# Performance work log

Measured on AMD Instinct MI355X. Metric: run time of the kernel, lower is better.

## Reference

```python
import jax, jax.numpy as jnp
import numpy as np

D_MODEL = 256
N_BINS = 11
# standard KNRM kernels: exact-match bin (mu=1, sigma=1e-3) + 10 soft bins
MUS = jnp.array([1.0, 0.9, 0.7, 0.5, 0.3, 0.1, -0.1, -0.3, -0.5, -0.7, -0.9], dtype=jnp.float32)
SIGMAS = jnp.array([1e-3] + [0.1] * 10, dtype=jnp.float32)


def _l2norm(x, eps=1e-10):
    # F.normalize(p=2, eps=1e-10): x / max(||x||, eps)
    n = jnp.sqrt(jnp.sum(x * x, axis=-1, keepdims=True))
    return x / jnp.maximum(n, eps)


def setup_inputs() -> dict:
    key = jax.random.key(0)
    ks = jax.random.split(key, 10)
    B, NB, Q, T, D = 64, 8, 32, 256, D_MODEL
    return {
        "word_atten": jax.random.uniform(ks[0], (B, NB, Q), dtype=jnp.float32),
        "hq": jax.random.normal(ks[1], (B, NB, Q, D), dtype=jnp.float32),
        "can": jax.random.normal(ks[2], (B, T, D), dtype=jnp.float32),
        "rep": jax.random.normal(ks[3], (B, NB, D), dtype=jnp.float32),
        "rep_cur": jax.random.normal(ks[4], (B, D), dtype=jnp.float32),
        "mask_hq": jnp.ones((B, NB, Q), dtype=jnp.float32),
        "mask_can": jnp.ones((B, T), dtype=jnp.float32),
        "mask_session": jnp.ones((B, NB), dtype=jnp.float32),
        "W_dense": jax.random.normal(ks[5], (N_BINS, 1), dtype=jnp.float32) * 0.3,
        "b_dense": jnp.zeros((1,), dtype=jnp.float32),
        "W_att": jax.random.normal(ks[6], (D, D), dtype=jnp.float32) * (1.0 / np.sqrt(D)),
        "b_att": jnp.zeros((D,), dtype=jnp.float32),
    }


def reference(word_atten, hq, can, rep, rep_cur, mask_hq, mask_can, mask_session,
              W_dense, b_dense, W_att, b_att):
    # cosine-similarity matrix: [B, NB, Q, T]
    hq_n = _l2norm(hq)
    can_n = _l2norm(can)
    matrix = jnp.einsum("bnqd,btd->bnqt", hq_n, can_n)

    # Gaussian kernel soft-binning: expand to [B, NB, Q, T, N_BINS]
    diff = matrix[..., None] - MUS  # broadcast over bins
    kern = jnp.exp(-(diff * diff) / (2.0 * SIGMAS * SIGMAS))
    kern = kern * mask_can[:, None, None, :, None]  # mask doc tokens
    pooling_sum = jnp.sum(kern, axis=3)  # [B, NB, Q, N_BINS]

    log_pool = jnp.log(jnp.clip(pooling_sum, 1e-10)) * 0.01
    log_pool = log_pool * mask_hq[..., None] * word_atten[..., None]
    pooled = jnp.sum(log_pool, axis=2)  # [B, NB, N_BINS]

    pooled = pooled * mask_session[..., None]

    # attention over session blocks (AttendAttention): scaled dot with projected current rep
    q = rep_cur @ W_att + b_att  # [B, D]
    scores = jnp.einsum("bnd,bd->bn", rep, q) / np.sqrt(D_MODEL).astype(np.float32)
    scores = jnp.where(mask_session > 0, scores, -1e9)
    attn = jax.nn.softmax(scores, axis=-1)  # [B, NB]

    score = jnp.tanh(pooled @ W_dense + b_dense).squeeze(-1)  # [B, NB]
    return jnp.sum(score * attn, axis=1)  # [B]
```

## Files before the change

kernel.cpp:

```cpp
#include <hip/hip_runtime.h>

#define B_ 64
#define NB_ 8
#define Q_ 32
#define T_ 256
#define D_ 256
#define NBINS 11

typedef __attribute__((ext_vector_type(8))) short bf16x8;
typedef __attribute__((ext_vector_type(4))) float f32x4;
typedef unsigned short ushort_t;
typedef unsigned int uint_t;

#define CANH_OFF 0u
#define CANL_OFF 8388608u

__device__ inline ushort_t bf16_rnd(float f) {
  uint_t u = __float_as_uint(f);
  return (ushort_t)((u + 0x8000u) >> 16);
}
__device__ inline uint_t pack2(ushort_t a, ushort_t b) {
  return (uint_t)a | ((uint_t)b << 16);
}

__global__ __launch_bounds__(256) void split_kernel(
    const float* __restrict__ can, uint4* __restrict__ canH,
    uint4* __restrict__ canL, float* __restrict__ out) {
  __shared__ __align__(16) ushort_t sm_hi[32 * 264];
  __shared__ __align__(16) ushort_t sm_lo[32 * 264];
  int blk = blockIdx.x;
  int tid = threadIdx.x;
  if (tid == 0 && blk < B_) out[blk] = 0.0f;
  int b = blk >> 3, ch = blk & 7;
  const float* src = can + ((size_t)b * T_ + ch * 32) * D_;
  int tilebase = b * 16 + ch * 2;

#pragma unroll
  for (int it = 0; it < 4; it++) {
    int flat = it * 2048 + tid * 8;
    int row = flat >> 8, col = flat & 255;
    const float* p = src + row * D_ + col;
    float4 x = reinterpret_cast<const float4*>(p)[0];
    float4 y = reinterpret_cast<const float4*>(p)[1];
    float s = x.x * x.x + x.y * x.y + x.z * x.z + x.w * x.w +
              y.x * y.x + y.y * y.y + y.z * y.z + y.w * y.w;
    s += __shfl_xor(s, 1);
    s += __shfl_xor(s, 2);
    s += __shfl_xor(s, 4);
    s += __shfl_xor(s, 8);
    s += __shfl_xor(s, 16);
    float inv = 1.0f / fmaxf(sqrtf(s), 1e-10f);
    float v[8] = {x.x, x.y, x.z, x.w, y.x, y.y, y.z, y.w};
    ushort_t h[8], l[8];
#pragma unroll
    for (int j = 0; j < 8; j++) {
      float sv = v[j] * inv;
      h[j] = bf16_rnd(sv);
      float hf = __uint_as_float(((uint_t)h[j]) << 16);
      l[j] = bf16_rnd(sv - hf);
    }
    uint4 ph = {pack2(h[0], h[1]), pack2(h[2], h[3]), pack2(h[4], h[5]),
                pack2(h[6], h[7])};
    uint4 pl = {pack2(l[0], l[1]), pack2(l[2], l[3]), pack2(l[4], l[5]),
                pack2(l[6], l[7])};
    *reinterpret_cast<uint4*>(&sm_hi[row * 264 + col]) = ph;
    *reinterpret_cast<uint4*>(&sm_lo[row * 264 + col]) = pl;
  }
  __syncthreads();
  int wv = tid >> 6, lane = tid & 63;
  int tl = wv >> 1, part = wv & 1;
  int lq = lane & 15, lk = lane >> 4;
  const ushort_t* smp = part ? sm_lo : sm_hi;
  uint4* dst = part ? canL : canH;
#pragma unroll
  for (int kk = 0; kk < 8; kk++) {
    const ushort_t* a = &smp[(tl * 16 + lq) * 264 + kk * 32 + lk * 8];
    dst[((size_t)(tilebase + tl) * 8 + kk) * 64 + lane] =
        *reinterpret_cast<const uint4*>(a);
  }
}

__global__ __launch_bounds__(256, 2) void pool_kernel(
    const float* __restrict__ hq, const uint4* __restrict__ canH,
    const uint4* __restrict__ canL, const float* __restrict__ mask_can,
    const float* __restrict__ word_atten, const float* __restrict__ mask_hq,
    const float* __restrict__ rep, const float* __restrict__ rep_cur,
    const float* __restrict__ mask_session, const float* __restrict__ W_dense,
    const float* __restrict__ b_dense, const float* __restrict__ W_att,
    const float* __restrict__ b_att, float* __restrict__ out) {
  __shared__ float smbuf[1331];
  float* partial = smbuf;
  float* lp_sm = smbuf + 704;
  float* qproj = smbuf + 1056;
  float* scores_sm = smbuf + 1312;
  float* pooled_sm = smbuf + 1320;

  const float mus[NBINS] = {1.0f, 0.9f, 0.7f, 0.5f, 0.3f, 0.1f,
                            -0.1f, -0.3f, -0.5f, -0.7f, -0.9f};
  const float nis2[NBINS] = {-5.0e5f, -50.f, -50.f, -50.f, -50.f, -50.f,
                             -50.f, -50.f, -50.f, -50.f, -50.f};

  int i = blockIdx.x;
  int b = i & 63;
  int nb = i >> 6;
  int outb = b * NB_ + nb;
  int tid = threadIdx.x;
  int wv = tid >> 6, lane = tid & 63;
  int lq = lane & 15, lk = lane >> 4;
  int mtile = wv & 1, tq = wv >> 1;

  const float* arow =
      hq + (size_t)outb * (Q_ * D_) + (size_t)(mtile * 16 + lq) * D_;
  float sumsq = 0.f;
#pragma unroll
  for (int kk = 0; kk < 8; kk++) {
    const float* p = arow + kk * 32 + lk * 8;
    float4 x = reinterpret_cast<const float4*>(p)[0];
    float4 y = reinterpret_cast<const float4*>(p)[1];
    sumsq += x.x * x.x + x.y * x.y + x.z * x.z + x.w * x.w +
             y.x * y.x + y.y * y.y + y.z * y.z + y.w * y.w;
  }
  sumsq += __shfl_xor(sumsq, 16);
  sumsq += __shfl_xor(sumsq, 32);
  float ainv = 1.0f / fmaxf(sqrtf(sumsq), 1e-10f);

  bf16x8 ah[8], al[8];
#pragma unroll
  for (int kk = 0; kk < 8; kk++) {
    const float* p = arow + kk * 32 + lk * 8;
    float4 x = reinterpret_cast<const float4*>(p)[0];
    float4 y = reinterpret_cast<const float4*>(p)[1];
    float v[8] = {x.x, x.y, x.z, x.w, y.x, y.y, y.z, y.w};
    union { bf16x8 v8; ushort_t u[8]; } H, L;
#pragma unroll
    for (int j = 0; j < 8; j++) {
      float s = v[j] * ainv;
      ushort_t h = bf16_rnd(s);
      float hf = __uint_as_float(((uint_t)h) << 16);
      H.u[j] = h;
      L.u[j] = bf16_rnd(s - hf);
    }
    ah[kk] = H.v8;
    al[kk] = L.v8;
  }

  float binacc[4][NBINS];
#pragma unroll
  for (int r = 0; r < 4; r++)
#pragma unroll
    for (int j = 0; j < NBINS; j++) binacc[r][j] = 0.0f;

  f32x4 accPrev;
  float mkPrev = 0.0f;

  {
    int tt = tq * 8;
    size_t bbase = (size_t)(b * 16 + tt) * 8 * 64 + lane;
    f32x4 acc = {0.f, 0.f, 0.f, 0.f};
#pragma unroll
    for (int kk = 0; kk < 8; kk++) {
      bf16x8 bh = *reinterpret_cast<const bf16x8*>(&canH[bbase + kk * 64]);
      bf16x8 bl = *reinterpret_cast<const bf16x8*>(&canL[bbase + kk * 64]);
      acc = __builtin_amdgcn_mfma_f32_16x16x32_bf16(ah[kk], bh, acc, 0, 0, 0);
      acc = __builtin_amdgcn_mfma_f32_16x16x32_bf16(al[kk], bh, acc, 0, 0, 0);
      acc = __builtin_amdgcn_mfma_f32_16x16x32_bf16(ah[kk], bl, acc, 0, 0, 0);
    }
    accPrev = acc;
    mkPrev = mask_can[b * T_ + tt * 16 + lq];
  }

  for (int ti = 1; ti < 8; ti++) {
    int tt = tq * 8 + ti;
    size_t bbase = (size_t)(b * 16 + tt) * 8 * 64 + lane;
    bf16x8 bh[8], bl[8];
#pragma unroll
    for (int kk = 0; kk < 8; kk++) {
      bh[kk] = *reinterpret_cast<const bf16x8*>(&canH[bbase + kk * 64]);
      bl[kk] = *reinterpret_cast<const bf16x8*>(&canL[bbase + kk * 64]);
    }
#pragma unroll
    for (int r = 0; r < 4; r++) {
      float v0 = accPrev[r];
#pragma unroll
      for (int j = 0; j < NBINS; j++) {
        float d0 = v0 - mus[j];
        binacc[r][j] += mkPrev * __expf(d0 * d0 * nis2[j]);
      }
    }
    f32x4 acc = {0.f, 0.f, 0.f, 0.f};
#pragma unroll
    for (int kk = 0; kk < 8; kk++) {
      acc = __builtin_amdgcn_mfma_f32_16x16x32_bf16(ah[kk], bh[kk], acc, 0, 0, 0);
      acc = __builtin_amdgcn_mfma_f32_16x16x32_bf16(al[kk], bh[kk], acc, 0, 0, 0);
      acc = __builtin_amdgcn_mfma_f32_16x16x32_bf16(ah[kk], bl[kk], acc, 0, 0, 0);
    }
    accPrev = acc;
    mkPrev = mask_can[b * T_ + tt * 16 + lq];
  }
#pragma unroll
  for (int r = 0; r < 4; r++) {
    float v0 = accPrev[r];
#pragma unroll
    for (int j = 0; j < NBINS; j++) {
      float d0 = v0 - mus[j];
      binacc[r][j] += mkPrev * __expf(d0 * d0 * nis2[j]);
    }
  }

#pragma unroll
  for (int r = 0; r < 4; r++)
#pragma unroll
    for (int j = 0; j < NBINS; j++) {
      float v = binacc[r][j];
      v += __shfl_xor(v, 1);
      v += __shfl_xor(v, 2);
      v += __shfl_xor(v, 4);
      v += __shfl_xor(v, 8);
      binacc[r][j] = v;
    }
  if (lq == 0) {
#pragma unroll
    for (int r = 0; r < 4; r++)
#pragma unroll
      for (int j = 0; j < NBINS; j++)
        partial[(wv * 16 + lk * 4 + r) * NBINS + j] = binacc[r][j];
  }
  __syncthreads();

  for (int idx = tid; idx < Q_ * NBINS; idx += 256) {
    int q = idx / NBINS;
    int j = idx - q * NBINS;
    int m = q >> 4, r16 = q & 15;
    float sum = partial[(m * 16 + r16) * NBINS + j] +
                partial[((2 + m) * 16 + r16) * NBINS + j];
    float wa = word_atten[outb * Q_ + q] * mask_hq[outb * Q_ + q];
    lp_sm[idx] = logf(fmaxf(sum, 1e-10f)) * 0.01f * wa;
  }

  {
    const float* rc = rep_cur + b * D_;
    float acc2 = b_att[tid];
    for (int k = 0; k < D_; k++) acc2 += rc[k] * W_att[k * D_ + tid];
    qproj[tid] = acc2;
  }
  __syncthreads();

  if (tid < NBINS) {
    float s = 0.f;
#pragma unroll
    for (int q = 0; q < Q_; q++) s += lp_sm[q * NBINS + tid];
    pooled_sm[tid] = s;
  }

  for (int nn = wv; nn < NB_; nn += 4) {
    const float* rp = rep + ((size_t)b * NB_ + nn) * D_;
    float4 r4 = reinterpret_cast<const float4*>(rp)[lane];
    float4 q4 = *reinterpret_cast<float4*>(&qproj[lane * 4]);
    float s = r4.x * q4.x + r4.y * q4.y + r4.z * q4.z + r4.w * q4.w;
#pragma unroll
    for (int off = 32; off > 0; off >>= 1) s += __shfl_down(s, off);
    if (lane == 0) scores_sm[nn] = s * 0.0625f;
  }
  __syncthreads();

  if (tid == 0) {
    float sc[NB_];
    float mx = -1e30f;
    for (int nn = 0; nn < NB_; nn++) {
      float s = (mask_session[b * NB_ + nn] > 0.f) ? scores_sm[nn] : -1e9f;
      sc[nn] = s;
      mx = fmaxf(mx, s);
    }
    float den = 0.f;
    for (int nn = 0; nn < NB_; nn++) {
      sc[nn] = __expf(sc[nn] - mx);
      den += sc[nn];
    }
    float ms = mask_session[b * NB_ + nb];
    float pw = b_dense[0];
#pragma unroll
    for (int j = 0; j < NBINS; j++) pw += pooled_sm[j] * ms * W_dense[j];
    float res = tanhf(pw) * (sc[nb] / den);
    atomicAdd(&out[b], res);
  }
}

extern "C" void kernel_launch(void* const* d_in, const int* in_sizes, int n_in,
                              void* d_out, int out_size, void* d_ws,
                              size_t ws_size, hipStream_t stream) {
  const float* word_atten = (const float*)d_in[0];
  const float* hq = (const float*)d_in[1];
  const float* can = (const float*)d_in[2];
  const float* rep = (const float*)d_in[3];
  const float* rep_cur = (const float*)d_in[4];
  const float* mask_hq = (const float*)d_in[5];
  const float* mask_can = (const float*)d_in[6];
  const float* mask_session = (const float*)d_in[7];
  const float* W_dense = (const float*)d_in[8];
  const float* b_dense = (const float*)d_in[9];
  const float* W_att = (const float*)d_in[10];
  const float* b_att = (const float*)d_in[11];
  float* out = (float*)d_out;

  char* ws = (char*)d_ws;
  uint4* canH = (uint4*)(ws + CANH_OFF);
  uint4* canL = (uint4*)(ws + CANL_OFF);

  hipLaunchKernelGGL(split_kernel, dim3(512), dim3(256), 0, stream, can, canH,
                     canL, out);
  hipLaunchKernelGGL(pool_kernel, dim3(B_ * NB_), dim3(256), 0, stream, hq,
                     canH, canL, mask_can, word_atten, mask_hq, rep, rep_cur,
                     mask_session, W_dense, b_dense, W_att, b_att, out);
}
```

Measured before the change: 127.1 us.

## Factor Gaussian bins via exponential recurrence and hoist attention to split kernel

Result: slower. 149.5 us (+17.6%).

```diff
diff --git a/kernel.cpp b/kernel.cpp
--- a/kernel.cpp
+++ b/kernel.cpp
@@ -14,6 +14,7 @@
 
 #define CANH_OFF 0u
 #define CANL_OFF 8388608u
+#define ATTN_OFF 16777216u
 
 __device__ inline ushort_t bf16_rnd(float f) {
   uint_t u = __float_as_uint(f);
@@ -23,11 +24,40 @@
   return (uint_t)a | ((uint_t)b << 16);
 }
 
+__device__ inline void kern_bins(float v, float mk, float* acc) {
+  float d0 = v - 1.0f;
+  acc[0] += mk * exp2f(d0 * d0 * -721347.52f);
+  float t = v - 0.1f;
+  float K = mk * exp2f(t * t * -72.134752f);
+  acc[5] += K;
+  float x = v * 28.853901f;
+  float eu = exp2f(x);
+  float ed = exp2f(-x);
+  const float E4 = 1.8315639e-2f;
+  const float E8 = 3.3546262e-4f;
+  const float E12 = 6.1442124e-6f;
+  const float E16 = 1.1253517e-7f;
+  float kd = K * ed;        acc[6] += kd;
+  kd = kd * ed * E4;        acc[7] += kd;
+  kd = kd * ed * E8;        acc[8] += kd;
+  kd = kd * ed * E12;       acc[9] += kd;
+  kd = kd * ed * E16;       acc[10] += kd;
+  float ku = K * eu * E4;   acc[4] += ku;
+  ku = ku * eu * E8;        acc[3] += ku;
+  ku = ku * eu * E12;       acc[2] += ku;
+  ku = ku * eu * E16;       acc[1] += ku;
+}
+
 __global__ __launch_bounds__(256) void split_kernel(
     const float* __restrict__ can, uint4* __restrict__ canH,
-    uint4* __restrict__ canL, float* __restrict__ out) {
+    uint4* __restrict__ canL, const float* __restrict__ rep,
+    const float* __restrict__ rep_cur, const float* __restrict__ mask_session,
+    const float* __restrict__ W_att, const float* __restrict__ b_att,
+    float* __restrict__ attn_out, float* __restrict__ out) {
   __shared__ __align__(16) ushort_t sm_hi[32 * 264];
   __shared__ __align__(16) ushort_t sm_lo[32 * 264];
+  __shared__ float qp_sm[256];
+  __shared__ float sc_sm[8];
   int blk = blockIdx.x;
   int tid = threadIdx.x;
   if (tid == 0 && blk < B_) out[blk] = 0.0f;
@@ -78,27 +108,55 @@
     dst[((size_t)(tilebase + tl) * 8 + kk) * 64 + lane] =
         *reinterpret_cast<const uint4*>(a);
   }
+
+  if (ch == 0) {
+    const float* rc = rep_cur + b * D_;
+    float acc2 = b_att[tid];
+#pragma unroll 8
+    for (int k = 0; k < D_; k++) acc2 += rc[k] * W_att[(size_t)k * D_ + tid];
+    qp_sm[tid] = acc2;
+    __syncthreads();
+    for (int nn = wv; nn < NB_; nn += 4) {
+      const float* rp = rep + ((size_t)b * NB_ + nn) * D_;
+      float4 r4 = reinterpret_cast<const float4*>(rp)[lane];
+      float4 q4 = *reinterpret_cast<const float4*>(&qp_sm[lane * 4]);
+      float s = r4.x * q4.x + r4.y * q4.y + r4.z * q4.z + r4.w * q4.w;
+#pragma unroll
+      for (int off = 32; off > 0; off >>= 1) s += __shfl_down(s, off);
+      if (lane == 0) sc_sm[nn] = s * 0.0625f;
+    }
+    __syncthreads();
+    if (tid == 0) {
+      float sc[NB_];
+      float mx = -1e30f;
+      for (int nn = 0; nn < NB_; nn++) {
+        float s = (mask_session[b * NB_ + nn] > 0.f) ? sc_sm[nn] : -1e9f;
+        sc[nn] = s;
+        mx = fmaxf(mx, s);
+      }
+      float den = 0.f;
+      for (int nn = 0; nn < NB_; nn++) {
+        sc[nn] = __expf(sc[nn] - mx);
+        den += sc[nn];
+      }
+      float invd = 1.0f / den;
+      for (int nn = 0; nn < NB_; nn++)
+        attn_out[b * NB_ + nn] = sc[nn] * invd;
+    }
+  }
 }
 
 __global__ __launch_bounds__(256, 2) void pool_kernel(
     const float* __restrict__ hq, const uint4* __restrict__ canH,
     const uint4* __restrict__ canL, const float* __restrict__ mask_can,
     const float* __restrict__ word_atten, const float* __restrict__ mask_hq,
-    const float* __restrict__ rep, const float* __restrict__ rep_cur,
     const float* __restrict__ mask_session, const float* __restrict__ W_dense,
-    const float* __restrict__ b_dense, const float* __restrict__ W_att,
-    const float* __restrict__ b_att, float* __restrict__ out) {
-  __shared__ float smbuf[1331];
+    const float* __restrict__ b_dense, const float* __restrict__ attn_ws,
+    float* __restrict__ out) {
+  __shared__ float smbuf[1067];
   float* partial = smbuf;
   float* lp_sm = smbuf + 704;
-  float* qproj = smbuf + 1056;
-  float* scores_sm = smbuf + 1312;
-  float* pooled_sm = smbuf + 1320;
-
-  const float mus[NBINS] = {1.0f, 0.9f, 0.7f, 0.5f, 0.3f, 0.1f,
-                            -0.1f, -0.3f, -0.5f, -0.7f, -0.9f};
-  const float nis2[NBINS] = {-5.0e5f, -50.f, -50.f, -50.f, -50.f, -50.f,
-                             -50.f, -50.f, -50.f, -50.f, -50.f};
+  float* pooled_sm = smbuf + 1056;
 
   int i = blockIdx.x;
   int b = i & 63;
@@ -179,14 +237,7 @@
       bl[kk] = *reinterpret_cast<const bf16x8*>(&canL[bbase + kk * 64]);
     }
 #pragma unroll
-    for (int r = 0; r < 4; r++) {
-      float v0 = accPrev[r];
-#pragma unroll
-      for (int j = 0; j < NBINS; j++) {
-        float d0 = v0 - mus[j];
-        binacc[r][j] += mkPrev * __expf(d0 * d0 * nis2[j]);
-      }
-    }
+    for (int r = 0; r < 4; r++) kern_bins(accPrev[r], mkPrev, binacc[r]);
     f32x4 acc = {0.f, 0.f, 0.f, 0.f};
 #pragma unroll
     for (int kk = 0; kk < 8; kk++) {
@@ -198,14 +249,8 @@
     mkPrev = mask_can[b * T_ + tt * 16 + lq];
   }
 #pragma unroll
-  for (int r = 0; r < 4; r++) {
-    float v0 = accPrev[r];
-#pragma unroll
-    for (int j = 0; j < NBINS; j++) {
-      float d0 = v0 - mus[j];
-      binacc[r][j] += mkPrev * __expf(d0 * d0 * nis2[j]);
-    }
-  }
+  for (int r = 0; r < 4; r++)
+    kern_bins(accPrev[r], mkPrev, binacc[r]);
 
 #pragma unroll
   for (int r = 0; r < 4; r++)
@@ -236,13 +281,6 @@
     float wa = word_atten[outb * Q_ + q] * mask_hq[outb * Q_ + q];
     lp_sm[idx] = logf(fmaxf(sum, 1e-10f)) * 0.01f * wa;
   }
-
-  {
-    const float* rc = rep_cur + b * D_;
-    float acc2 = b_att[tid];
-    for (int k = 0; k < D_; k++) acc2 += rc[k] * W_att[k * D_ + tid];
-    qproj[tid] = acc2;
-  }
   __syncthreads();
 
   if (tid < NBINS) {
@@ -251,36 +289,12 @@
     for (int q = 0; q < Q_; q++) s += lp_sm[q * NBINS + tid];
     pooled_sm[tid] = s;
   }
-
-  for (int nn = wv; nn < NB_; nn += 4) {
-    const float* rp = rep + ((size_t)b * NB_ + nn) * D_;
-    float4 r4 = reinterpret_cast<const float4*>(rp)[lane];
-    float4 q4 = *reinterpret_cast<float4*>(&qproj[lane * 4]);
-    float s = r4.x * q4.x + r4.y * q4.y + r4.z * q4.z + r4.w * q4.w;
-#pragma unroll
-    for (int off = 32; off > 0; off >>= 1) s += __shfl_down(s, off);
-    if (lane == 0) scores_sm[nn] = s * 0.0625f;
-  }
-  __syncthreads();
-
   if (tid == 0) {
-    float sc[NB_];
-    float mx = -1e30f;
-    for (int nn = 0; nn < NB_; nn++) {
-      float s = (mask_session[b * NB_ + nn] > 0.f) ? scores_sm[nn] : -1e9f;
-      sc[nn] = s;
-      mx = fmaxf(mx, s);
-    }
-    float den = 0.f;
-    for (int nn = 0; nn < NB_; nn++) {
-      sc[nn] = __expf(sc[nn] - mx);
-      den += sc[nn];
-    }
-    float ms = mask_session[b * NB_ + nb];
+    float ms = mask_session[outb];
     float pw = b_dense[0];
 #pragma unroll
     for (int j = 0; j < NBINS; j++) pw += pooled_sm[j] * ms * W_dense[j];
-    float res = tanhf(pw) * (sc[nb] / den);
+    float res = tanhf(pw) * attn_ws[outb];
     atomicAdd(&out[b], res);
   }
 }
@@ -305,10 +319,12 @@
   char* ws = (char*)d_ws;
   uint4* canH = (uint4*)(ws + CANH_OFF);
   uint4* canL = (uint4*)(ws + CANL_OFF);
+  float* attn_ws = (float*)(ws + ATTN_OFF);
 
   hipLaunchKernelGGL(split_kernel, dim3(512), dim3(256), 0, stream, can, canH,
-                     canL, out);
+                     canL, rep, rep_cur, mask_session, W_att, b_att, attn_ws,
+                     out);
   hipLaunchKernelGGL(pool_kernel, dim3(B_ * NB_), dim3(256), 0, stream, hq,
-                     canH, canL, mask_can, word_atten, mask_hq, rep, rep_cur,
-                     mask_session, W_dense, b_dense, W_att, b_att, out);
-}
+                     canH, canL, mask_can, word_atten, mask_hq, mask_session,
+                     W_dense, b_dense, attn_ws, out);
+}
```

## Split pooling across T chunks, pre-split hq, add finish kernel

Applied to the files above, without the earlier changes.

Result: slower. 139.7 us (+10.0%).

```diff
diff --git a/kernel.cpp b/kernel.cpp
--- a/kernel.cpp
+++ b/kernel.cpp
@@ -14,6 +14,9 @@
 
 #define CANH_OFF 0u
 #define CANL_OFF 8388608u
+#define HQH_OFF 16777216u
+#define HQL_OFF 25165824u
+#define PSUM_OFF 33554432u
 
 __device__ inline ushort_t bf16_rnd(float f) {
   uint_t u = __float_as_uint(f);
@@ -23,17 +26,46 @@
   return (uint_t)a | ((uint_t)b << 16);
 }
 
+__device__ inline void bins_acc(f32x4 acc, float mk, float binacc[4][NBINS]) {
+  const float mus[NBINS] = {1.0f, 0.9f, 0.7f, 0.5f, 0.3f, 0.1f,
+                            -0.1f, -0.3f, -0.5f, -0.7f, -0.9f};
+  const float nis2[NBINS] = {-5.0e5f, -50.f, -50.f, -50.f, -50.f, -50.f,
+                             -50.f, -50.f, -50.f, -50.f, -50.f};
+#pragma unroll
+  for (int r = 0; r < 4; r++) {
+    float v0 = acc[r];
+#pragma unroll
+    for (int j = 0; j < NBINS; j++) {
+      float d0 = v0 - mus[j];
+      binacc[r][j] += mk * __expf(d0 * d0 * nis2[j]);
+    }
+  }
+}
+
 __global__ __launch_bounds__(256) void split_kernel(
-    const float* __restrict__ can, uint4* __restrict__ canH,
-    uint4* __restrict__ canL, float* __restrict__ out) {
+    const float* __restrict__ can, const float* __restrict__ hq,
+    uint4* __restrict__ canH, uint4* __restrict__ canL,
+    uint4* __restrict__ hqH, uint4* __restrict__ hqL) {
   __shared__ __align__(16) ushort_t sm_hi[32 * 264];
   __shared__ __align__(16) ushort_t sm_lo[32 * 264];
   int blk = blockIdx.x;
   int tid = threadIdx.x;
-  if (tid == 0 && blk < B_) out[blk] = 0.0f;
-  int b = blk >> 3, ch = blk & 7;
-  const float* src = can + ((size_t)b * T_ + ch * 32) * D_;
-  int tilebase = b * 16 + ch * 2;
+  const float* src;
+  uint4 *dH, *dL;
+  int tilebase;
+  if (blk < 512) {
+    int b = blk >> 3, ch = blk & 7;
+    src = can + ((size_t)b * T_ + ch * 32) * D_;
+    dH = canH;
+    dL = canL;
+    tilebase = b * 16 + ch * 2;
+  } else {
+    int outb = blk - 512;
+    src = hq + (size_t)outb * (Q_ * D_);
+    dH = hqH;
+    dL = hqL;
+    tilebase = outb * 2;
+  }
 
 #pragma unroll
   for (int it = 0; it < 4; it++) {
@@ -71,7 +103,7 @@
   int tl = wv >> 1, part = wv & 1;
   int lq = lane & 15, lk = lane >> 4;
   const ushort_t* smp = part ? sm_lo : sm_hi;
-  uint4* dst = part ? canL : canH;
+  uint4* dst = part ? dL : dH;
 #pragma unroll
   for (int kk = 0; kk < 8; kk++) {
     const ushort_t* a = &smp[(tl * 16 + lq) * 264 + kk * 32 + lk * 8];
@@ -81,68 +113,32 @@
 }
 
 __global__ __launch_bounds__(256, 2) void pool_kernel(
-    const float* __restrict__ hq, const uint4* __restrict__ canH,
-    const uint4* __restrict__ canL, const float* __restrict__ mask_can,
-    const float* __restrict__ word_atten, const float* __restrict__ mask_hq,
-    const float* __restrict__ rep, const float* __restrict__ rep_cur,
-    const float* __restrict__ mask_session, const float* __restrict__ W_dense,
-    const float* __restrict__ b_dense, const float* __restrict__ W_att,
-    const float* __restrict__ b_att, float* __restrict__ out) {
-  __shared__ float smbuf[1331];
-  float* partial = smbuf;
-  float* lp_sm = smbuf + 704;
-  float* qproj = smbuf + 1056;
-  float* scores_sm = smbuf + 1312;
-  float* pooled_sm = smbuf + 1320;
-
-  const float mus[NBINS] = {1.0f, 0.9f, 0.7f, 0.5f, 0.3f, 0.1f,
-                            -0.1f, -0.3f, -0.5f, -0.7f, -0.9f};
-  const float nis2[NBINS] = {-5.0e5f, -50.f, -50.f, -50.f, -50.f, -50.f,
-                             -50.f, -50.f, -50.f, -50.f, -50.f};
+    const uint4* __restrict__ hqH, const uint4* __restrict__ hqL,
+    const uint4* __restrict__ canH, const uint4* __restrict__ canL,
+    const float* __restrict__ mask_can, float* __restrict__ psum) {
+  __shared__ float partial[4 * 16 * NBINS];
 
   int i = blockIdx.x;
   int b = i & 63;
-  int nb = i >> 6;
+  int rest = i >> 6;
+  int nb = rest & 7, ts = rest >> 3;
   int outb = b * NB_ + nb;
   int tid = threadIdx.x;
   int wv = tid >> 6, lane = tid & 63;
   int lq = lane & 15, lk = lane >> 4;
   int mtile = wv & 1, tq = wv >> 1;
 
-  const float* arow =
-      hq + (size_t)outb * (Q_ * D_) + (size_t)(mtile * 16 + lq) * D_;
-  float sumsq = 0.f;
-#pragma unroll
-  for (int kk = 0; kk < 8; kk++) {
-    const float* p = arow + kk * 32 + lk * 8;
-    float4 x = reinterpret_cast<const float4*>(p)[0];
-    float4 y = reinterpret_cast<const float4*>(p)[1];
-    sumsq += x.x * x.x + x.y * x.y + x.z * x.z + x.w * x.w +
-             y.x * y.x + y.y * y.y + y.z * y.z + y.w * y.w;
-  }
-  sumsq += __shfl_xor(sumsq, 16);
-  sumsq += __shfl_xor(sumsq, 32);
-  float ainv = 1.0f / fmaxf(sqrtf(sumsq), 1e-10f);
-
   bf16x8 ah[8], al[8];
-#pragma unroll
-  for (int kk = 0; kk < 8; kk++) {
-    const float* p = arow + kk * 32 + lk * 8;
-    float4 x = reinterpret_cast<const float4*>(p)[0];
-    float4 y = reinterpret_cast<const float4*>(p)[1];
-    float v[8] = {x.x, x.y, x.z, x.w, y.x, y.y, y.z, y.w};
-    union { bf16x8 v8; ushort_t u[8]; } H, L;
-#pragma unroll
-    for (int j = 0; j < 8; j++) {
-      float s = v[j] * ainv;
-      ushort_t h = bf16_rnd(s);
-      float hf = __uint_as_float(((uint_t)h) << 16);
-      H.u[j] = h;
-      L.u[j] = bf16_rnd(s - hf);
-    }
-    ah[kk] = H.v8;
-    al[kk] = L.v8;
-  }
+  size_t abase = (size_t)(outb * 2 + mtile) * 512 + lane;
+#pragma unroll
+  for (int kk = 0; kk < 8; kk++) {
+    ah[kk] = *reinterpret_cast<const bf16x8*>(&hqH[abase + kk * 64]);
+    al[kk] = *reinterpret_cast<const bf16x8*>(&hqL[abase + kk * 64]);
+  }
+
+  int t0 = ts * 4 + tq * 2;
+  float mk0 = mask_can[b * T_ + (t0 + 0) * 16 + lq];
+  float mk1 = mask_can[b * T_ + (t0 + 1) * 16 + lq];
 
   float binacc[4][NBINS];
 #pragma unroll
@@ -150,62 +146,31 @@
 #pragma unroll
     for (int j = 0; j < NBINS; j++) binacc[r][j] = 0.0f;
 
-  f32x4 accPrev;
-  float mkPrev = 0.0f;
-
-  {
-    int tt = tq * 8;
-    size_t bbase = (size_t)(b * 16 + tt) * 8 * 64 + lane;
-    f32x4 acc = {0.f, 0.f, 0.f, 0.f};
-#pragma unroll
-    for (int kk = 0; kk < 8; kk++) {
-      bf16x8 bh = *reinterpret_cast<const bf16x8*>(&canH[bbase + kk * 64]);
-      bf16x8 bl = *reinterpret_cast<const bf16x8*>(&canL[bbase + kk * 64]);
-      acc = __builtin_amdgcn_mfma_f32_16x16x32_bf16(ah[kk], bh, acc, 0, 0, 0);
-      acc = __builtin_amdgcn_mfma_f32_16x16x32_bf16(al[kk], bh, acc, 0, 0, 0);
-      acc = __builtin_amdgcn_mfma_f32_16x16x32_bf16(ah[kk], bl, acc, 0, 0, 0);
-    }
-    accPrev = acc;
-    mkPrev = mask_can[b * T_ + tt * 16 + lq];
-  }
-
-  for (int ti = 1; ti < 8; ti++) {
-    int tt = tq * 8 + ti;
-    size_t bbase = (size_t)(b * 16 + tt) * 8 * 64 + lane;
-    bf16x8 bh[8], bl[8];
-#pragma unroll
-    for (int kk = 0; kk < 8; kk++) {
-      bh[kk] = *reinterpret_cast<const bf16x8*>(&canH[bbase + kk * 64]);
-      bl[kk] = *reinterpret_cast<const bf16x8*>(&canL[bbase + kk * 64]);
-    }
-#pragma unroll
-    for (int r = 0; r < 4; r++) {
-      float v0 = accPrev[r];
-#pragma unroll
-      for (int j = 0; j < NBINS; j++) {
-        float d0 = v0 - mus[j];
-        binacc[r][j] += mkPrev * __expf(d0 * d0 * nis2[j]);
-      }
-    }
-    f32x4 acc = {0.f, 0.f, 0.f, 0.f};
-#pragma unroll
-    for (int kk = 0; kk < 8; kk++) {
-      acc = __builtin_amdgcn_mfma_f32_16x16x32_bf16(ah[kk], bh[kk], acc, 0, 0, 0);
-      acc = __builtin_amdgcn_mfma_f32_16x16x32_bf16(al[kk], bh[kk], acc, 0, 0, 0);
-      acc = __builtin_amdgcn_mfma_f32_16x16x32_bf16(ah[kk], bl[kk], acc, 0, 0, 0);
-    }
-    accPrev = acc;
-    mkPrev = mask_can[b * T_ + tt * 16 + lq];
-  }
-#pragma unroll
-  for (int r = 0; r < 4; r++) {
-    float v0 = accPrev[r];
-#pragma unroll
-    for (int j = 0; j < NBINS; j++) {
-      float d0 = v0 - mus[j];
-      binacc[r][j] += mkPrev * __expf(d0 * d0 * nis2[j]);
-    }
-  }
+  size_t bbase = (size_t)(b * 16 + t0) * 512 + lane;
+  f32x4 acc0 = {0.f, 0.f, 0.f, 0.f};
+#pragma unroll
+  for (int kk = 0; kk < 8; kk++) {
+    bf16x8 bh = *reinterpret_cast<const bf16x8*>(&canH[bbase + kk * 64]);
+    bf16x8 bl = *reinterpret_cast<const bf16x8*>(&canL[bbase + kk * 64]);
+    acc0 = __builtin_amdgcn_mfma_f32_16x16x32_bf16(ah[kk], bh, acc0, 0, 0, 0);
+    acc0 = __builtin_amdgcn_mfma_f32_16x16x32_bf16(al[kk], bh, acc0, 0, 0, 0);
+    acc0 = __builtin_amdgcn_mfma_f32_16x16x32_bf16(ah[kk], bl, acc0, 0, 0, 0);
+  }
+  bf16x8 bh1[8], bl1[8];
+#pragma unroll
+  for (int kk = 0; kk < 8; kk++) {
+    bh1[kk] = *reinterpret_cast<const bf16x8*>(&canH[bbase + 512 + kk * 64]);
+    bl1[kk] = *reinterpret_cast<const bf16x8*>(&canL[bbase + 512 + kk * 64]);
+  }
+  bins_acc(acc0, mk0, binacc);
+  f32x4 acc1 = {0.f, 0.f, 0.f, 0.f};
+#pragma unroll
+  for (int kk = 0; kk < 8; kk++) {
+    acc1 = __builtin_amdgcn_mfma_f32_16x16x32_bf16(ah[kk], bh1[kk], acc1, 0, 0, 0);
+    acc1 = __builtin_amdgcn_mfma_f32_16x16x32_bf16(al[kk], bh1[kk], acc1, 0, 0, 0);
+    acc1 = __builtin_amdgcn_mfma_f32_16x16x32_bf16(ah[kk], bl1[kk], acc1, 0, 0, 0);
+  }
+  bins_acc(acc1, mk1, binacc);
 
 #pragma unroll
   for (int r = 0; r < 4; r++)
@@ -231,24 +196,60 @@
     int q = idx / NBINS;
     int j = idx - q * NBINS;
     int m = q >> 4, r16 = q & 15;
-    float sum = partial[(m * 16 + r16) * NBINS + j] +
-                partial[((2 + m) * 16 + r16) * NBINS + j];
-    float wa = word_atten[outb * Q_ + q] * mask_hq[outb * Q_ + q];
-    lp_sm[idx] = logf(fmaxf(sum, 1e-10f)) * 0.01f * wa;
-  }
-
-  {
+    float s = partial[((0 + m) * 16 + r16) * NBINS + j] +
+              partial[((2 + m) * 16 + r16) * NBINS + j];
+    psum[((size_t)(outb * 4 + ts)) * (Q_ * NBINS) + idx] = s;
+  }
+}
+
+__global__ __launch_bounds__(256) void finish_kernel(
+    const float* __restrict__ psum, const float* __restrict__ word_atten,
+    const float* __restrict__ mask_hq, const float* __restrict__ rep,
+    const float* __restrict__ rep_cur, const float* __restrict__ mask_session,
+    const float* __restrict__ W_dense, const float* __restrict__ b_dense,
+    const float* __restrict__ W_att, const float* __restrict__ b_att,
+    float* __restrict__ out) {
+  __shared__ float qproj[256];
+  __shared__ float lp_sm[NB_ * Q_ * NBINS];
+  __shared__ float pooled_sm[NB_ * NBINS];
+  __shared__ float scores_sm[NB_];
+
+  int b = blockIdx.x;
+  int tid = threadIdx.x;
+  int wv = tid >> 6, lane = tid & 63;
+
+  if (wv < 2) {
     const float* rc = rep_cur + b * D_;
-    float acc2 = b_att[tid];
-    for (int k = 0; k < D_; k++) acc2 += rc[k] * W_att[k * D_ + tid];
-    qproj[tid] = acc2;
+    float a0 = b_att[tid], a1 = b_att[tid + 128];
+#pragma unroll 8
+    for (int k = 0; k < D_; k++) {
+      float r = rc[k];
+      a0 += r * W_att[k * D_ + tid];
+      a1 += r * W_att[k * D_ + tid + 128];
+    }
+    qproj[tid] = a0;
+    qproj[tid + 128] = a1;
+  } else {
+    int t2 = tid - 128;
+    for (int idx = t2; idx < NB_ * Q_ * NBINS; idx += 128) {
+      int nn = idx / (Q_ * NBINS);
+      int rem = idx - nn * (Q_ * NBINS);
+      int q = rem / NBINS;
+      int outb = b * NB_ + nn;
+      const float* pp = psum + ((size_t)outb * 4) * (Q_ * NBINS) + rem;
+      float s = pp[0] + pp[Q_ * NBINS] + pp[2 * Q_ * NBINS] +
+                pp[3 * Q_ * NBINS];
+      float wa = word_atten[outb * Q_ + q] * mask_hq[outb * Q_ + q];
+      lp_sm[idx] = logf(fmaxf(s, 1e-10f)) * 0.01f * wa;
+    }
   }
   __syncthreads();
 
-  if (tid < NBINS) {
+  if (tid < NB_ * NBINS) {
+    int nn = tid / NBINS, j = tid - nn * NBINS;
     float s = 0.f;
 #pragma unroll
-    for (int q = 0; q < Q_; q++) s += lp_sm[q * NBINS + tid];
+    for (int q = 0; q < Q_; q++) s += lp_sm[(nn * Q_ + q) * NBINS + j];
     pooled_sm[tid] = s;
   }
 
@@ -276,12 +277,17 @@
       sc[nn] = __expf(sc[nn] - mx);
       den += sc[nn];
     }
-    float ms = mask_session[b * NB_ + nb];
-    float pw = b_dense[0];
-#pragma unroll
-    for (int j = 0; j < NBINS; j++) pw += pooled_sm[j] * ms * W_dense[j];
-    float res = tanhf(pw) * (sc[nb] / den);
-    atomicAdd(&out[b], res);
+    float invd = 1.0f / den;
+    float res = 0.f;
+    for (int nn = 0; nn < NB_; nn++) {
+      float ms = mask_session[b * NB_ + nn];
+      float pw = b_dense[0];
+#pragma unroll
+      for (int j = 0; j < NBINS; j++)
+        pw += pooled_sm[nn * NBINS + j] * ms * W_dense[j];
+      res += tanhf(pw) * sc[nn] * invd;
+    }
+    out[b] = res;
   }
 }
 
@@ -305,10 +311,15 @@
   char* ws = (char*)d_ws;
   uint4* canH = (uint4*)(ws + CANH_OFF);
   uint4* canL = (uint4*)(ws + CANL_OFF);
-
-  hipLaunchKernelGGL(split_kernel, dim3(512), dim3(256), 0, stream, can, canH,
-                     canL, out);
-  hipLaunchKernelGGL(pool_kernel, dim3(B_ * NB_), dim3(256), 0, stream, hq,
-                     canH, canL, mask_can, word_atten, mask_hq, rep, rep_cur,
-                     mask_session, W_dense, b_dense, W_att, b_att, out);
-}
+  uint4* hqH = (uint4*)(ws + HQH_OFF);
+  uint4* hqL = (uint4*)(ws + HQL_OFF);
+  float* psum = (float*)(ws + PSUM_OFF);
+
+  hipLaunchKernelGGL(split_kernel, dim3(1024), dim3(256), 0, stream, can, hq,
+                     canH, canL, hqH, hqL);
+  hipLaunchKernelGGL(pool_kernel, dim3(2048), dim3(256), 0, stream, hqH, hqL,
+                     canH, canL, mask_can, psum);
+  hipLaunchKernelGGL(finish_kernel, dim3(B_), dim3(256), 0, stream, psum,
+                     word_atten, mask_hq, rep, rep_cur, mask_session, W_dense,
+                     b_dense, W_att, b_att, out);
+}
```

## Stage candidate tiles through double-buffered LDS via async global-to-LDS loads

Applied to the files above, without the earlier changes.

After: 131.5 us. +3.5%, slower.

```diff
diff --git a/kernel.cpp b/kernel.cpp
--- a/kernel.cpp
+++ b/kernel.cpp
@@ -21,6 +21,12 @@
 }
 __device__ inline uint_t pack2(ushort_t a, ushort_t b) {
   return (uint_t)a | ((uint_t)b << 16);
+}
+
+__device__ inline void gld_lds16(const void* g, void* l) {
+  __builtin_amdgcn_global_load_lds(
+      (const __attribute__((address_space(1))) void*)g,
+      (__attribute__((address_space(3))) void*)l, 16, 0, 0);
 }
 
 __global__ __launch_bounds__(256) void split_kernel(
@@ -88,6 +94,7 @@
     const float* __restrict__ mask_session, const float* __restrict__ W_dense,
     const float* __restrict__ b_dense, const float* __restrict__ W_att,
     const float* __restrict__ b_att, float* __restrict__ out) {
+  __shared__ __align__(16) ushort_t ldsB[2][2][2][4096];
   __shared__ float smbuf[1331];
   float* partial = smbuf;
   float* lp_sm = smbuf + 704;
@@ -144,6 +151,17 @@
     al[kk] = L.v8;
   }
 
+  const uint4* srcP = mtile ? canL : canH;
+  ushort_t* sb = &ldsB[tq][0][0][0];
+  const int BUF = 2 * 4096;
+  int myPart = mtile * 4096;
+  size_t tbase = (size_t)(b * 16 + tq * 8) * 512 + lane;
+
+#pragma unroll
+  for (int kk = 0; kk < 8; kk++)
+    gld_lds16(&srcP[tbase + kk * 64], &sb[myPart + kk * 512]);
+  __syncthreads();
+
   float binacc[4][NBINS];
 #pragma unroll
   for (int r = 0; r < 4; r++)
@@ -152,50 +170,45 @@
 
   f32x4 accPrev;
   float mkPrev = 0.0f;
-
-  {
-    int tt = tq * 8;
-    size_t bbase = (size_t)(b * 16 + tt) * 8 * 64 + lane;
+  int bufoff = 0;
+
+  for (int ti = 0; ti < 8; ti++) {
+    if (ti < 7) {
+      int ob = bufoff ^ BUF;
+#pragma unroll
+      for (int kk = 0; kk < 8; kk++)
+        gld_lds16(&srcP[tbase + (size_t)(ti + 1) * 512 + kk * 64],
+                  &sb[ob + myPart + kk * 512]);
+    }
+    if (ti > 0) bins_acc_body: {
+      ;
+    }
+    if (ti > 0) {
+#pragma unroll
+      for (int r = 0; r < 4; r++) {
+        float v0 = accPrev[r];
+#pragma unroll
+        for (int j = 0; j < NBINS; j++) {
+          float d0 = v0 - mus[j];
+          binacc[r][j] += mkPrev * __expf(d0 * d0 * nis2[j]);
+        }
+      }
+    }
     f32x4 acc = {0.f, 0.f, 0.f, 0.f};
 #pragma unroll
     for (int kk = 0; kk < 8; kk++) {
-      bf16x8 bh = *reinterpret_cast<const bf16x8*>(&canH[bbase + kk * 64]);
-      bf16x8 bl = *reinterpret_cast<const bf16x8*>(&canL[bbase + kk * 64]);
+      bf16x8 bh = *reinterpret_cast<const bf16x8*>(
+          &sb[bufoff + 0 + kk * 512 + lane * 8]);
+      bf16x8 bl = *reinterpret_cast<const bf16x8*>(
+          &sb[bufoff + 4096 + kk * 512 + lane * 8]);
       acc = __builtin_amdgcn_mfma_f32_16x16x32_bf16(ah[kk], bh, acc, 0, 0, 0);
       acc = __builtin_amdgcn_mfma_f32_16x16x32_bf16(al[kk], bh, acc, 0, 0, 0);
       acc = __builtin_amdgcn_mfma_f32_16x16x32_bf16(ah[kk], bl, acc, 0, 0, 0);
     }
     accPrev = acc;
-    mkPrev = mask_can[b * T_ + tt * 16 + lq];
-  }
-
-  for (int ti = 1; ti < 8; ti++) {
-    int tt = tq * 8 + ti;
-    size_t bbase = (size_t)(b * 16 + tt) * 8 * 64 + lane;
-    bf16x8 bh[8], bl[8];
-#pragma unroll
-    for (int kk = 0; kk < 8; kk++) {
-      bh[kk] = *reinterpret_cast<const bf16x8*>(&canH[bbase + kk * 64]);
-      bl[kk] = *reinterpret_cast<const bf16x8*>(&canL[bbase + kk * 64]);
-    }
-#pragma unroll
-    for (int r = 0; r < 4; r++) {
-      float v0 = accPrev[r];
-#pragma unroll
-      for (int j = 0; j < NBINS; j++) {
-        float d0 = v0 - mus[j];
-        binacc[r][j] += mkPrev * __expf(d0 * d0 * nis2[j]);
-      }
-    }
-    f32x4 acc = {0.f, 0.f, 0.f, 0.f};
-#pragma unroll
-    for (int kk = 0; kk < 8; kk++) {
-      acc = __builtin_amdgcn_mfma_f32_16x16x32_bf16(ah[kk], bh[kk], acc, 0, 0, 0);
-      acc = __builtin_amdgcn_mfma_f32_16x16x32_bf16(al[kk], bh[kk], acc, 0, 0, 0);
-      acc = __builtin_amdgcn_mfma_f32_16x16x32_bf16(ah[kk], bl[kk], acc, 0, 0, 0);
-    }
-    accPrev = acc;
-    mkPrev = mask_can[b * T_ + tt * 16 + lq];
+    mkPrev = mask_can[b * T_ + (tq * 8 + ti) * 16 + lq];
+    __syncthreads();
+    bufoff ^= BUF;
   }
 #pragma unroll
   for (int r = 0; r < 4; r++) {
```
